# Kernel optimization log

Measured on AMD Instinct MI355X. Metric: run time of the kernel, lower is better.

The kernel has to match this reference:

```python
import jax, jax.numpy as jnp
import numpy as np

B, S, D = 4, 2048, 2048
NH, NKV = 16, 4
HD = D // NH  # 128


def setup_inputs() -> dict:
    key = jax.random.key(0)
    ks = jax.random.split(key, 6)
    sd = 1.0 / np.sqrt(D)
    return {
        "x": jax.random.normal(ks[0], (B, S, D), jnp.float32),
        "cos": jax.random.normal(ks[1], (1, 1, S, HD), jnp.float32),
        "sin": jax.random.normal(ks[2], (1, 1, S, HD), jnp.float32),
        "wq_w": jax.random.normal(ks[3], (D, D), jnp.float32) * sd,
        "wk_w": jax.random.normal(ks[4], (NKV * HD, D), jnp.float32) * sd,
        "wv_w": jax.random.normal(ks[5], (NKV * HD, D), jnp.float32) * sd,
        "start_pos": 0,
    }


def _rotate_half(t):
    h = t.shape[-1] // 2
    return jnp.concatenate([-t[..., h:], t[..., :h]], axis=-1)


def reference(x, cos, sin, wq_w, wk_w, wv_w, start_pos):
    b, s, d = x.shape
    n_rep = NH // NKV
    q = (x @ wq_w.T).reshape(b, s, NH, HD).transpose(0, 2, 1, 3)      # [b,H,s,hd]
    k = (x @ wk_w.T).reshape(b, s, NKV, HD).transpose(0, 2, 1, 3)     # [b,Hk,s,hd]
    v = (x @ wv_w.T).reshape(b, s, NKV, HD).transpose(0, 2, 1, 3)
    # rotary
    q = q * cos + _rotate_half(q) * sin
    k = k * cos + _rotate_half(k) * sin
    # repeat_kv
    k = jnp.repeat(k, n_rep, axis=1)   # [b,H,s,hd]
    v = jnp.repeat(v, n_rep, axis=1)
    scores = jnp.einsum("bhqd,bhkd->bhqk", q, k) / jnp.sqrt(jnp.float32(HD))
    causal = jnp.tril(jnp.ones((s, s), dtype=bool))
    scores = jnp.where(causal, scores, jnp.float32(-jnp.inf))
    w = jax.nn.softmax(scores, axis=-1)
    out = jnp.einsum("bhqk,bhkd->bhqd", w, v)
    return out.transpose(0, 2, 1, 3).reshape(b, s, d)
```

## Files before the change

kernel.cpp:

```cpp
#include <hip/hip_runtime.h>
#include <hip/hip_bf16.h>
#include <math.h>

#define B_ 4
#define S_ 2048
#define D_ 2048
#define NH_ 16
#define NKV_ 4
#define HD_ 128

typedef short bf16x8 __attribute__((ext_vector_type(8)));
typedef float f32x4 __attribute__((ext_vector_type(4)));
typedef unsigned u32x4 __attribute__((ext_vector_type(4)));
typedef __hip_bfloat16 bf16;

#define ASYNC_CP16(gp, lp)                                                    \
  __builtin_amdgcn_global_load_lds(                                           \
      (const __attribute__((address_space(1))) unsigned int*)(gp),            \
      (__attribute__((address_space(3))) unsigned int*)(lp), 16, 0, 0)

__global__ __launch_bounds__(256) void cvt_kernel(const float* __restrict__ in,
                                                  bf16* __restrict__ out, int n4) {
  int i = blockIdx.x * 256 + threadIdx.x;
  if (i >= n4) return;
  float4 v = ((const float4*)in)[i];
  union { ushort4 u; bf16 h[4]; } o;
  o.h[0] = __float2bfloat16(v.x);
  o.h[1] = __float2bfloat16(v.y);
  o.h[2] = __float2bfloat16(v.z);
  o.h[3] = __float2bfloat16(v.w);
  ((ushort4*)out)[i] = o.u;
}

__global__ __launch_bounds__(256) void cvt_w_kernel(const float* __restrict__ wq,
                                                    const float* __restrict__ wk,
                                                    const float* __restrict__ wv,
                                                    bf16* __restrict__ out) {
  int i = blockIdx.x * 256 + threadIdx.x;
  const float4* src; int off;
  if (i < 1048576)      { src = (const float4*)wq; off = i; }
  else if (i < 1310720) { src = (const float4*)wk; off = i - 1048576; }
  else                  { src = (const float4*)wv; off = i - 1310720; }
  float4 v = src[off];
  union { ushort4 u; bf16 h[4]; } o;
  o.h[0] = __float2bfloat16(v.x);
  o.h[1] = __float2bfloat16(v.y);
  o.h[2] = __float2bfloat16(v.z);
  o.h[3] = __float2bfloat16(v.w);
  ((ushort4*)out)[i] = o.u;
}

__global__ __launch_bounds__(512, 2) void gemm_qkv(
    const bf16* __restrict__ A, const bf16* __restrict__ W,
    bf16* __restrict__ qr, bf16* __restrict__ kr, bf16* __restrict__ vlin,
    const float* __restrict__ cosp, const float* __restrict__ sinp,
    float qscale) {
  __shared__ __align__(16) bf16 As[3][256 * 64];
  __shared__ __align__(16) bf16 Bs[3][128 * 64];
  const int tid = threadIdx.x;
  const int lane = tid & 63, wave = tid >> 6;
  const int wm = (wave >> 1) * 64, wn = (wave & 1) * 64;
  const int m0 = blockIdx.x * 256;
  const int hblk = blockIdx.y;
  const int n0 = hblk * 128;
  const int quad = lane >> 4, c = lane & 15;
  const int K = 2048;
  const int T = K / 64;

  f32x4 acc[4][4] = {};

  const int srow = wave * 8 + (lane >> 3);
  const int gcol = ((lane & 7) ^ ((lane >> 3) & 7)) * 8;
  const bf16* Aptr = A + (size_t)(m0 + srow) * K + gcol;
  const bf16* Bptr = W + (size_t)(n0 + srow) * K + gcol;

#define STAGE_A(kb_, buf_, i_)                                                \
  ASYNC_CP16(Aptr + (size_t)(i_) * 64 * K + (kb_),                            \
             &As[buf_][((i_) * 64 + wave * 8) * 64])
#define STAGE_B(kb_, buf_, i_)                                                \
  ASYNC_CP16(Bptr + (size_t)(i_) * 64 * K + (kb_),                            \
             &Bs[buf_][((i_) * 64 + wave * 8) * 64])

  {
#pragma unroll
    for (int i = 0; i < 4; i++) STAGE_A(0, 0, i);
#pragma unroll
    for (int i = 0; i < 2; i++) STAGE_B(0, 0, i);
#pragma unroll
    for (int i = 0; i < 4; i++) STAGE_A(64, 1, i);
#pragma unroll
    for (int i = 0; i < 2; i++) STAGE_B(64, 1, i);
    asm volatile("s_waitcnt vmcnt(6)" ::: "memory");
    __builtin_amdgcn_s_barrier();
    __builtin_amdgcn_sched_barrier(0);
  }

  int cur = 0, stg = 2;
#pragma unroll 1
  for (int t = 0; t < T; ++t) {
    const bf16* Asc = &As[cur][0];
    const bf16* Bsc = &Bs[cur][0];
    const bool st = (t + 2) < T;
    const size_t kb2 = (size_t)(t + 2) * 64;

    {
      const int slot = (quad ^ (c & 7)) * 8;
      bf16x8 af[4], bfr[4];
#pragma unroll
      for (int q4 = 0; q4 < 4; q4++) {
        af[q4]  = *(const bf16x8*)(&Asc[(wm + q4 * 16 + c) * 64 + slot]);
        bfr[q4] = *(const bf16x8*)(&Bsc[(wn + q4 * 16 + c) * 64 + slot]);
      }
      if (st) { STAGE_A(kb2, stg, 0); STAGE_A(kb2, stg, 1); STAGE_A(kb2, stg, 2); }
      __builtin_amdgcn_sched_barrier(0);
      __builtin_amdgcn_s_barrier();
      __builtin_amdgcn_s_setprio(1);
#pragma unroll
      for (int mt = 0; mt < 4; mt++)
#pragma unroll
        for (int nt = 0; nt < 4; nt++)
          acc[mt][nt] = __builtin_amdgcn_mfma_f32_16x16x32_bf16(
              af[mt], bfr[nt], acc[mt][nt], 0, 0, 0);
      __builtin_amdgcn_s_setprio(0);
      __builtin_amdgcn_s_barrier();
      __builtin_amdgcn_sched_barrier(0);
    }
    {
      const int slot = ((4 + quad) ^ (c & 7)) * 8;
      bf16x8 af[4], bfr[4];
#pragma unroll
      for (int q4 = 0; q4 < 4; q4++) {
        af[q4]  = *(const bf16x8*)(&Asc[(wm + q4 * 16 + c) * 64 + slot]);
        bfr[q4] = *(const bf16x8*)(&Bsc[(wn + q4 * 16 + c) * 64 + slot]);
      }
      if (st) { STAGE_A(kb2, stg, 3); STAGE_B(kb2, stg, 0); STAGE_B(kb2, stg, 1); }
      __builtin_amdgcn_sched_barrier(0);
      __builtin_amdgcn_s_barrier();
      __builtin_amdgcn_s_setprio(1);
#pragma unroll
      for (int mt = 0; mt < 4; mt++)
#pragma unroll
        for (int nt = 0; nt < 4; nt++)
          acc[mt][nt] = __builtin_amdgcn_mfma_f32_16x16x32_bf16(
              af[mt], bfr[nt], acc[mt][nt], 0, 0, 0);
      __builtin_amdgcn_s_setprio(0);
      if (t + 1 < T) {
        if (st) asm volatile("s_waitcnt vmcnt(6)" ::: "memory");
        else    asm volatile("s_waitcnt vmcnt(0)" ::: "memory");
      }
      __builtin_amdgcn_s_barrier();
      __builtin_amdgcn_sched_barrier(0);
    }
    cur = (cur == 2) ? 0 : cur + 1;
    stg = (stg == 2) ? 0 : stg + 1;
  }
#undef STAGE_A
#undef STAGE_B

  __syncthreads();

  if (hblk >= 20) {
    const int colb = (hblk - 20) * 128 + wn;
#pragma unroll
    for (int mt = 0; mt < 4; mt++)
#pragma unroll
      for (int reg = 0; reg < 4; reg++) {
        int m = m0 + wm + mt * 16 + quad * 4 + reg;
        bf16* row = vlin + (size_t)m * (NKV_ * HD_) + colb;
#pragma unroll
        for (int nt = 0; nt < 4; nt++)
          row[nt * 16 + c] = __float2bfloat16(acc[mt][nt][reg]);
      }
  } else {
    float* Sc = (float*)&As[0][0];
    if (wn) {
#pragma unroll
      for (int mt = 0; mt < 4; mt++)
#pragma unroll
        for (int reg = 0; reg < 4; reg++) {
          int lr = wm + mt * 16 + quad * 4 + reg;
#pragma unroll
          for (int nt = 0; nt < 4; nt++)
            Sc[lr * 64 + nt * 16 + c] = acc[mt][nt][reg];
        }
    }
    __syncthreads();
    if (!wn) {
      const float scale = (hblk < 16) ? qscale : 1.0f;
#pragma unroll
      for (int mt = 0; mt < 4; mt++)
#pragma unroll
        for (int reg = 0; reg < 4; reg++) {
          int lr = wm + mt * 16 + quad * 4 + reg;
          int m = m0 + lr;
          int b = m >> 11, s = m & 2047;
          const float* cr = cosp + s * HD_;
          const float* sn = sinp + s * HD_;
          bf16* orow = (hblk < 16)
              ? qr + ((size_t)(b * NH_ + hblk) * S_ + s) * HD_
              : kr + ((size_t)(b * NKV_ + (hblk - 16)) * S_ + s) * HD_;
#pragma unroll
          for (int nt = 0; nt < 4; nt++) {
            int d1 = nt * 16 + c, d2 = d1 + 64;
            float q1 = acc[mt][nt][reg];
            float q2 = Sc[lr * 64 + d1];
            float o1 = (q1 * cr[d1] - q2 * sn[d1]) * scale;
            float o2 = (q2 * cr[d2] + q1 * sn[d2]) * scale;
            orow[d1] = __float2bfloat16(o1);
            orow[d2] = __float2bfloat16(o2);
          }
        }
    }
  }
}

__global__ __launch_bounds__(256) void v_transpose(const bf16* __restrict__ in,
                                                   int instride,
                                                   bf16* __restrict__ out) {
  __shared__ __align__(16) bf16 tile[64][HD_ + 8];
  int bidx = blockIdx.x;
  int st = bidx & 31;
  int kv = (bidx >> 5) & 3;
  int b = bidx >> 7;
  int s0 = st * 64;
  int t = threadIdx.x;
  {
    int row = t >> 2;
    int colb = (t & 3) * 32;
#pragma unroll
    for (int i = 0; i < 4; i++) {
      int col = colb + i * 8;
      *(uint4*)(&tile[row][col]) = *(const uint4*)(
          &in[(size_t)(b * S_ + s0 + row) * instride + kv * HD_ + col]);
    }
  }
  __syncthreads();
  int sl = t & 63, hb = t >> 6;
#pragma unroll
  for (int i = 0; i < 32; i++) {
    int hd = i * 4 + hb;
    out[((size_t)(b * NKV_ + kv) * HD_ + hd) * S_ + s0 + sl] = tile[sl][hd];
  }
}

__device__ __forceinline__ void attn_step2(
    const bf16* __restrict__ Ks, const bf16* __restrict__ Vs,
    bf16* __restrict__ PsA, bf16* __restrict__ PsB,
    const bf16x8* qfA, const bf16x8* qfB, f32x4* oA, f32x4* oB,
    float& mA, float& lA, float& mB, float& lB,
    bool diagA, bool diagB, int kb, int qbA, int quad, int c) {
  f32x4 sA[4] = {}, sB[4] = {};
#pragma unroll
  for (int kt = 0; kt < 4; kt++) {
    const int slot = ((kt * 4 + quad) ^ (c & 7)) * 8;
#pragma unroll
    for (int mt = 0; mt < 4; mt++) {
      bf16x8 kf = *(const bf16x8*)(&Ks[(mt * 16 + c) * 128 + slot]);
      sA[mt] = __builtin_amdgcn_mfma_f32_16x16x32_bf16(kf, qfA[kt], sA[mt], 0, 0, 0);
      sB[mt] = __builtin_amdgcn_mfma_f32_16x16x32_bf16(kf, qfB[kt], sB[mt], 0, 0, 0);
    }
  }
  if (diagA) {
    const int qg = qbA + c;
#pragma unroll
    for (int mt = 0; mt < 4; mt++)
#pragma unroll
      for (int r = 0; r < 4; r++)
        if (kb + mt * 16 + quad * 4 + r > qg) sA[mt][r] = -INFINITY;
  }
  if (diagB) {
    const int qg = qbA + 16 + c;
#pragma unroll
    for (int mt = 0; mt < 4; mt++)
#pragma unroll
      for (int r = 0; r < 4; r++)
        if (kb + mt * 16 + quad * 4 + r > qg) sB[mt][r] = -INFINITY;
  }

#define SOFTMAX_PACK(sacc, m_i, l_i, o, Psw)                                  \
  do {                                                                        \
    f32x4 mx4 = __builtin_elementwise_max(                                    \
        __builtin_elementwise_max(sacc[0], sacc[1]),                          \
        __builtin_elementwise_max(sacc[2], sacc[3]));                         \
    float mx = fmaxf(fmaxf(mx4[0], mx4[1]), fmaxf(mx4[2], mx4[3]));          \
    mx = fmaxf(mx, __shfl_xor(mx, 16, 64));                                   \
    mx = fmaxf(mx, __shfl_xor(mx, 32, 64));                                   \
    if (!__all(mx - m_i <= 8.0f)) {                                           \
      const float mnew = fmaxf(m_i, mx);                                      \
      const float alpha = exp2f(m_i - mnew);                                  \
      m_i = mnew;                                                             \
      l_i *= alpha;                                                           \
      f32x4 av;                                                               \
      av[0] = __shfl(alpha, quad * 4 + 0, 64);                                \
      av[1] = __shfl(alpha, quad * 4 + 1, 64);                                \
      av[2] = __shfl(alpha, quad * 4 + 2, 64);                                \
      av[3] = __shfl(alpha, quad * 4 + 3, 64);                                \
      _Pragma("unroll")                                                       \
      for (int nt = 0; nt < 8; nt++) o[nt] *= av;                             \
    }                                                                         \
    const f32x4 mn4 = {m_i, m_i, m_i, m_i};                                   \
    f32x4 rs4 = {0.f, 0.f, 0.f, 0.f};                                         \
    _Pragma("unroll")                                                         \
    for (int mt = 0; mt < 4; mt++) {                                          \
      f32x4 e = sacc[mt] - mn4;                                               \
      f32x4 p;                                                                \
      p[0] = exp2f(e[0]); p[1] = exp2f(e[1]);                                 \
      p[2] = exp2f(e[2]); p[3] = exp2f(e[3]);                                 \
      rs4 += p;                                                               \
      u32x4 u = __builtin_bit_cast(u32x4, p) + 0x8000u;                       \
      uint2 pk;                                                               \
      pk.x = __builtin_amdgcn_perm(u[1], u[0], 0x07060302u);                  \
      pk.y = __builtin_amdgcn_perm(u[3], u[2], 0x07060302u);                  \
      const int pslot = mt * 2 + (quad >> 1);                                 \
      *(uint2*)(&Psw[c * 64 + ((pslot ^ (c & 7)) << 3) + (quad & 1) * 4]) = pk; \
    }                                                                         \
    float rs = (rs4[0] + rs4[1]) + (rs4[2] + rs4[3]);                         \
    rs += __shfl_xor(rs, 16, 64);                                             \
    rs += __shfl_xor(rs, 32, 64);                                             \
    l_i += rs;                                                                \
  } while (0)

  SOFTMAX_PACK(sA, mA, lA, oA, PsA);
  SOFTMAX_PACK(sB, mB, lB, oB, PsB);
#undef SOFTMAX_PACK

#pragma unroll
  for (int kk = 0; kk < 2; kk++) {
    const int psl = (((kk * 4 + quad) ^ (c & 7)) << 3);
    bf16x8 pfA = *(const bf16x8*)(&PsA[c * 64 + psl]);
    bf16x8 pfB = *(const bf16x8*)(&PsB[c * 64 + psl]);
    const int slot = ((kk * 4 + quad) ^ (c & 7)) * 8;
#pragma unroll
    for (int nt = 0; nt < 8; nt++) {
      bf16x8 vf = *(const bf16x8*)(&Vs[(nt * 16 + c) * 64 + slot]);
      oA[nt] = __builtin_amdgcn_mfma_f32_16x16x32_bf16(pfA, vf, oA[nt], 0, 0, 0);
      oB[nt] = __builtin_amdgcn_mfma_f32_16x16x32_bf16(pfB, vf, oB[nt], 0, 0, 0);
    }
  }
}

__global__ __launch_bounds__(256, 2) void attn_kernel(const bf16* __restrict__ Q,
                                                      const bf16* __restrict__ Kr,
                                                      const bf16* __restrict__ Vt,
                                                      float* __restrict__ O) {
  __shared__ __align__(16) bf16 Ks[2][64 * 128];
  __shared__ __align__(16) bf16 Vs[2][128 * 64];
  __shared__ __align__(16) bf16 Ps[4][2][16 * 64];

  const int tid = threadIdx.x, lane = tid & 63, wave = tid >> 6;
  const int quad = lane >> 4, c = lane & 15;
  const int j = blockIdx.x;
  const int bh = blockIdx.y;
  const int b = bh >> 4, h = bh & 15, kv = h >> 2;
  bf16* PsA = &Ps[wave][0][0];
  bf16* PsB = &Ps[wave][1][0];

  const bf16* kbase = Kr + (size_t)(b * NKV_ + kv) * S_ * HD_;
  const bf16* vbase = Vt + (size_t)(b * NKV_ + kv) * HD_ * S_;

  int koff[4], voff;
  {
    const int kl = lane >> 4;
    const int ks = lane & 15;
#pragma unroll
    for (int i = 0; i < 4; i++) {
      int r = wave * 16 + i * 4 + kl;
      koff[i] = r * HD_ + ((ks ^ (r & 7)) * 8);
    }
    const int vl = lane >> 3;
    const int vs = lane & 7;
    voff = (wave * 32 + vl) * S_ + ((vs ^ (vl & 7)) * 8);
  }

#define STAGE(kb_, buf_)                                                      \
  do {                                                                        \
    _Pragma("unroll")                                                         \
    for (int i_ = 0; i_ < 4; i_++) {                                          \
      ASYNC_CP16(kbase + (size_t)(kb_) * HD_ + koff[i_],                      \
                 &Ks[buf_][(wave * 16 + i_ * 4) * 128]);                      \
      ASYNC_CP16(vbase + (kb_) + voff + (size_t)(i_ * 8) * S_,                \
                 &Vs[buf_][(wave * 32 + i_ * 8) * 64]);                       \
    }                                                                         \
  } while (0)

#pragma unroll 1
  for (int pass = 0; pass < 2; ++pass) {
    const int jj = pass ? (15 - j) : j;
    const int q0 = jj * 128;
    const int qb = q0 + wave * 32;
    const int nsteps = 2 * jj + 2;

    bf16x8 qfA[4], qfB[4];
    {
      const bf16* qpA = Q + ((size_t)(b * NH_ + h) * S_ + qb + c) * HD_;
      const bf16* qpB = qpA + (size_t)16 * HD_;
#pragma unroll
      for (int kt = 0; kt < 4; kt++) {
        qfA[kt] = *(const bf16x8*)(qpA + kt * 32 + quad * 8);
        qfB[kt] = *(const bf16x8*)(qpB + kt * 32 + quad * 8);
      }
    }
    f32x4 oA[8] = {}, oB[8] = {};
    float mA = -INFINITY, lA = 0.f, mB = -INFINITY, lB = 0.f;

    __syncthreads();
    STAGE(0, 0);
    int cur = 0;

#pragma unroll 1
    for (int it = 0; it < nsteps; ++it) {
      const int kb = it * 64;
      __syncthreads();
      if (it + 1 < nsteps) STAGE((it + 1) * 64, cur ^ 1);
      if (kb <= qb + 31)
        attn_step2(&Ks[cur][0], &Vs[cur][0], PsA, PsB, qfA, qfB, oA, oB,
                   mA, lA, mB, lB, kb + 63 > qb, kb + 63 > qb + 16,
                   kb, qb, quad, c);
      cur ^= 1;
    }

    float* obase = O + (size_t)b * S_ * D_ + (size_t)h * HD_;
    {
      float inv[4];
#pragma unroll
      for (int r = 0; r < 4; r++) inv[r] = 1.0f / __shfl(lA, quad * 4 + r, 64);
#pragma unroll
      for (int nt = 0; nt < 8; nt++)
#pragma unroll
        for (int r = 0; r < 4; r++)
          obase[(size_t)(qb + quad * 4 + r) * D_ + nt * 16 + c] = oA[nt][r] * inv[r];
    }
    {
      float inv[4];
#pragma unroll
      for (int r = 0; r < 4; r++) inv[r] = 1.0f / __shfl(lB, quad * 4 + r, 64);
#pragma unroll
      for (int nt = 0; nt < 8; nt++)
#pragma unroll
        for (int r = 0; r < 4; r++)
          obase[(size_t)(qb + 16 + quad * 4 + r) * D_ + nt * 16 + c] = oB[nt][r] * inv[r];
    }
  }
#undef STAGE
}

extern "C" void kernel_launch(void* const* d_in, const int* in_sizes, int n_in,
                              void* d_out, int out_size, void* d_ws, size_t ws_size,
                              hipStream_t stream) {
  const float* x    = (const float*)d_in[0];
  const float* cosp = (const float*)d_in[1];
  const float* sinp = (const float*)d_in[2];
  const float* wq   = (const float*)d_in[3];
  const float* wk   = (const float*)d_in[4];
  const float* wv   = (const float*)d_in[5];
  float* out = (float*)d_out;

  char* ws = (char*)d_ws;
  const size_t MB = 1024 * 1024;
  bf16* xb    = (bf16*)(ws + 0);
  bf16* wqkvb = (bf16*)(ws + 32 * MB);
  bf16* qr    = (bf16*)(ws + 44 * MB);
  bf16* kr    = (bf16*)(ws + 76 * MB);
  bf16* vlin  = (bf16*)(ws + 84 * MB);
  bf16* vt    = (bf16*)(ws + 92 * MB);

  cvt_kernel<<<16384, 256, 0, stream>>>(x, xb, 4194304);
  cvt_w_kernel<<<6144, 256, 0, stream>>>(wq, wk, wv, wqkvb);

  const float qscale = 1.4426950408889634f / 11.313708498984761f;
  gemm_qkv<<<dim3(32, 24), 512, 0, stream>>>(xb, wqkvb, qr, kr, vlin,
                                             cosp, sinp, qscale);

  v_transpose<<<512, 256, 0, stream>>>(vlin, NKV_ * HD_, vt);

  attn_kernel<<<dim3(8, 64), 256, 0, stream>>>(qr, kr, vt, out);
}
```

Before: 378.1 us.

## Replace async global-to-LDS copies with register-staged prefetch in attention loop

The K/V tile staging no longer uses global_load_lds async copies. Instead each thread loads the next tile into registers before computing the current step and writes it to the swizzled shared-memory buffer after the compute. A sched_barrier keeps the loads issued ahead of the MFMA work, so global latency should overlap with compute. The cost is extra VGPRs for the staging registers, which could lower occupancy, plus explicit LDS store instructions.

```diff
diff --git a/kernel.cpp b/kernel.cpp
--- a/kernel.cpp
+++ b/kernel.cpp
@@ -358,28 +358,34 @@
   const bf16* kbase = Kr + (size_t)(b * NKV_ + kv) * S_ * HD_;
   const bf16* vbase = Vt + (size_t)(b * NKV_ + kv) * HD_ * S_;
 
-  int koff[4], voff;
-  {
-    const int kl = lane >> 4;
-    const int ks = lane & 15;
-#pragma unroll
-    for (int i = 0; i < 4; i++) {
-      int r = wave * 16 + i * 4 + kl;
-      koff[i] = r * HD_ + ((ks ^ (r & 7)) * 8);
-    }
-    const int vl = lane >> 3;
-    const int vs = lane & 7;
-    voff = (wave * 32 + vl) * S_ + ((vs ^ (vl & 7)) * 8);
-  }
-
-#define STAGE(kb_, buf_)                                                      \
+  int kgo[4], klo[4], vgo[4], vlo[4];
+#pragma unroll
+  for (int i = 0; i < 4; i++) {
+    int kc = i * 256 + tid;
+    int krow = kc >> 4, kch = kc & 15;
+    kgo[i] = krow * HD_ + kch * 8;
+    klo[i] = krow * 128 + ((kch ^ (krow & 7)) * 8);
+    int vc = i * 256 + tid;
+    int vrow = vc >> 3, vch = vc & 7;
+    vgo[i] = vrow * S_ + vch * 8;
+    vlo[i] = vrow * 64 + ((vch ^ (vrow & 7)) * 8);
+  }
+
+  uint4 kreg[4], vreg[4];
+#define ISSUE(kb_)                                                            \
   do {                                                                        \
     _Pragma("unroll")                                                         \
     for (int i_ = 0; i_ < 4; i_++) {                                          \
-      ASYNC_CP16(kbase + (size_t)(kb_) * HD_ + koff[i_],                      \
-                 &Ks[buf_][(wave * 16 + i_ * 4) * 128]);                      \
-      ASYNC_CP16(vbase + (kb_) + voff + (size_t)(i_ * 8) * S_,                \
-                 &Vs[buf_][(wave * 32 + i_ * 8) * 64]);                       \
+      kreg[i_] = *(const uint4*)(kbase + (size_t)(kb_) * HD_ + kgo[i_]);      \
+      vreg[i_] = *(const uint4*)(vbase + (kb_) + vgo[i_]);                    \
+    }                                                                         \
+  } while (0)
+#define WRITE(buf_)                                                           \
+  do {                                                                        \
+    _Pragma("unroll")                                                         \
+    for (int i_ = 0; i_ < 4; i_++) {                                          \
+      *(uint4*)(&Ks[buf_][klo[i_]]) = kreg[i_];                               \
+      *(uint4*)(&Vs[buf_][vlo[i_]]) = vreg[i_];                               \
     }                                                                         \
   } while (0)
 
@@ -390,6 +396,9 @@
     const int qb = q0 + wave * 32;
     const int nsteps = 2 * jj + 2;
 
+    __syncthreads();
+    ISSUE(0);
+
     bf16x8 qfA[4], qfB[4];
     {
       const bf16* qpA = Q + ((size_t)(b * NH_ + h) * S_ + qb + c) * HD_;
@@ -403,19 +412,21 @@
     f32x4 oA[8] = {}, oB[8] = {};
     float mA = -INFINITY, lA = 0.f, mB = -INFINITY, lB = 0.f;
 
-    __syncthreads();
-    STAGE(0, 0);
+    WRITE(0);
     int cur = 0;
 
 #pragma unroll 1
     for (int it = 0; it < nsteps; ++it) {
       const int kb = it * 64;
       __syncthreads();
-      if (it + 1 < nsteps) STAGE((it + 1) * 64, cur ^ 1);
+      const bool stg = (it + 1 < nsteps);
+      if (stg) ISSUE((it + 1) * 64);
+      __builtin_amdgcn_sched_barrier(0);
       if (kb <= qb + 31)
         attn_step2(&Ks[cur][0], &Vs[cur][0], PsA, PsB, qfA, qfB, oA, oB,
                    mA, lA, mB, lB, kb + 63 > qb, kb + 63 > qb + 16,
                    kb, qb, quad, c);
+      if (stg) WRITE(cur ^ 1);
       cur ^= 1;
     }
 
@@ -441,7 +452,8 @@
           obase[(size_t)(qb + 16 + quad * 4 + r) * D_ + nt * 16 + c] = oB[nt][r] * inv[r];
     }
   }
-#undef STAGE
+#undef ISSUE
+#undef WRITE
 }
 
 extern "C" void kernel_launch(void* const* d_in, const int* in_sizes, int n_in,
```

Result: slower. 450.1 us (+19.0%).
